# Performance work log

Measured on AMD Instinct MI355X. Metric: run time of the kernel, lower is better.

Reference implementation:

```python
import jax, jax.numpy as jnp
import numpy as np

N_NODES = 200000
N_EDGES = 6400000
N_LAYERS = 3
Z_DIM = 4  # 2*4 + 1 + 3 == 12 == Linear in_features


def setup_inputs() -> dict:
    key = jax.random.key(0)
    ks = jax.random.split(key, 7)
    z = jax.random.normal(ks[0], (N_NODES, Z_DIM), dtype=jnp.float32)
    r = jax.random.uniform(ks[1], (N_EDGES, 1), dtype=jnp.float32)
    r_hat = jax.random.normal(ks[2], (N_EDGES, 3), dtype=jnp.float32)
    # Per-layer Linear(12, 1) weights and biases, stacked over layers.
    W = jax.random.normal(ks[3], (N_LAYERS, 1, 12), dtype=jnp.float32) * (1.0 / np.sqrt(12.0))
    b = jnp.zeros((N_LAYERS, 1), dtype=jnp.float32)
    src = jax.random.randint(ks[4], (N_EDGES,), 0, N_NODES, dtype=jnp.int32)
    dst = jax.random.randint(ks[5], (N_EDGES,), 0, N_NODES, dtype=jnp.int32)
    return {"z": z, "r": r, "r_hat": r_hat, "W": W, "b": b, "src": src, "dst": dst}


def reference(z, r, r_hat, W, b, src, dst):
    # batch['x'] = batch['z'].copy()
    x = z
    n_nodes = z.shape[0]
    for i in range(W.shape[0]):
        # Per-edge gather + concat -> [E, 12]
        inpt = jnp.concatenate([z[src], z[dst], r, r_hat], axis=-1)
        # Tiny Linear(12, 1) -> per-edge scalar message [E, 1]
        msg = inpt @ W[i].T + b[i]
        # Scatter-sum messages onto destination nodes, residual update.
        agg = jax.ops.segment_sum(msg, dst, num_segments=n_nodes)  # [N, 1]
        z = z + agg  # broadcast over the 4 node features
    return z, x
```

## Files before the change

### kernel.cpp

```cpp
#include <hip/hip_runtime.h>

#define N_NODES 200000
#define N_EDGES 6400000
#define K_BUCKETS 256
#define BUCKET 784
#define NSB 1600
#define CHUNK 4000

__device__ __forceinline__ unsigned short f2bf(float x) {
    unsigned u = __float_as_uint(x);
    u += 0x7fffu + ((u >> 16) & 1u);
    return (unsigned short)(u >> 16);
}
__device__ __forceinline__ float bf2f(unsigned short h) {
    return __uint_as_float((unsigned)h << 16);
}


__global__ __launch_bounds__(256) void copy_x_prep(const float4* __restrict__ z,
                                                   float4* __restrict__ x_out,
                                                   float* __restrict__ Scum)
{
    int n = blockIdx.x * 256 + threadIdx.x;
    if (n < N_NODES) { x_out[n] = z[n]; Scum[n] = 0.0f; }
}

__global__ __launch_bounds__(256) void hist_kernel(const int* __restrict__ dst,
                                                   int* __restrict__ counts_T)
{
    __shared__ int cnt[K_BUCKETS];
    int tid = threadIdx.x, sb = blockIdx.x;
    cnt[tid] = 0;
    __syncthreads();
    int e0 = sb * CHUNK;
    for (int i = tid; i < CHUNK; i += 256)
        atomicAdd(&cnt[dst[e0 + i] / BUCKET], 1);
    __syncthreads();
    counts_T[(size_t)tid * NSB + sb] = cnt[tid];
}

__global__ __launch_bounds__(256) void scan_cols(const int* __restrict__ counts_T,
                                                 int* __restrict__ baseRel_T,
                                                 int* __restrict__ tot)
{
    __shared__ int buf[256];
    __shared__ int carry_s;
    int k = blockIdx.x, tid = threadIdx.x;
    if (tid == 0) carry_s = 0;
    __syncthreads();
    const int* col = counts_T + (size_t)k * NSB;
    int* outc = baseRel_T + (size_t)k * NSB;
    for (int base = 0; base < NSB; base += 256) {
        int idx = base + tid;
        int v = (idx < NSB) ? col[idx] : 0;
        buf[tid] = v;
        __syncthreads();
        for (int off = 1; off < 256; off <<= 1) {
            int t = (tid >= off) ? buf[tid - off] : 0;
            __syncthreads();
            buf[tid] += t;
            __syncthreads();
        }
        int incl = buf[tid];
        if (idx < NSB) outc[idx] = carry_s + incl - v;
        __syncthreads();
        if (tid == 255) carry_s += incl;
        __syncthreads();
    }
    if (tid == 255) tot[k] = carry_s;
}

__global__ __launch_bounds__(256) void scan_tot(const int* __restrict__ tot,
                                                int* __restrict__ bstart)
{
    __shared__ int buf[256];
    int tid = threadIdx.x;
    int v = tot[tid];
    buf[tid] = v;
    __syncthreads();
    for (int off = 1; off < 256; off <<= 1) {
        int t = (tid >= off) ? buf[tid - off] : 0;
        __syncthreads();
        buf[tid] += t;
        __syncthreads();
    }
    bstart[tid] = buf[tid] - v;
    if (tid == 255) bstart[256] = buf[255];
}

__global__ __launch_bounds__(256) void scatter_kernel(
    const int* __restrict__ src, const int* __restrict__ dst,
    const float* __restrict__ r, const float* __restrict__ r_hat,
    const float* __restrict__ W, const float* __restrict__ b,
    const int* __restrict__ baseRel_T, const int* __restrict__ bstart,
    int* __restrict__ packedA,
    unsigned short* __restrict__ c0a, unsigned short* __restrict__ c1a,
    unsigned short* __restrict__ c2a)
{
    __shared__ int cnt[K_BUCKETS];
    __shared__ int cur[K_BUCKETS];
    __shared__ int delta[K_BUCKETS];
    __shared__ int scanbuf[256];
    __shared__ int            lpack[CHUNK];
    __shared__ unsigned short lc0[CHUNK];
    __shared__ unsigned short lc1[CHUNK];
    __shared__ unsigned short lc2[CHUNK];
    __shared__ unsigned char  skb[CHUNK];

    int tid = threadIdx.x, sb = blockIdx.x;
    cnt[tid] = 0;
    __syncthreads();
    int e0 = sb * CHUNK;

    for (int i = tid; i < CHUNK; i += 256)
        atomicAdd(&cnt[dst[e0 + i] / BUCKET], 1);
    __syncthreads();

    int v = cnt[tid];
    scanbuf[tid] = v;
    __syncthreads();
    for (int off = 1; off < 256; off <<= 1) {
        int t = (tid >= off) ? scanbuf[tid - off] : 0;
        __syncthreads();
        scanbuf[tid] += t;
        __syncthreads();
    }
    int localBase = scanbuf[tid] - v;
    int gBase = bstart[tid] + baseRel_T[(size_t)tid * NSB + sb];
    delta[tid] = gBase - localBase;
    cur[tid] = localBase;
    __syncthreads();

    float w8_0 = W[8],  w9_0 = W[9],  w10_0 = W[10], w11_0 = W[11], b0 = b[0];
    float w8_1 = W[20], w9_1 = W[21], w10_1 = W[22], w11_1 = W[23], b1 = b[1];
    float w8_2 = W[32], w9_2 = W[33], w10_2 = W[34], w11_2 = W[35], b2 = b[2];

    for (int i = tid; i < CHUNK; i += 256) {
        int e = e0 + i;
        int d = dst[e];
        int k = d / BUCKET;
        int dl = d - k * BUCKET;
        int slot = atomicAdd(&cur[k], 1);
        int sn = src[e];
        float rv = r[e];
        size_t he = 3 * (size_t)e;
        float h0 = r_hat[he], h1 = r_hat[he + 1], h2 = r_hat[he + 2];
        lpack[slot] = (sn << 10) | dl;
        lc0[slot] = f2bf(w8_0 * rv + w9_0 * h0 + w10_0 * h1 + w11_0 * h2 + b0);
        lc1[slot] = f2bf(w8_1 * rv + w9_1 * h0 + w10_1 * h1 + w11_1 * h2 + b1);
        lc2[slot] = f2bf(w8_2 * rv + w9_2 * h0 + w10_2 * h1 + w11_2 * h2 + b2);
        skb[slot] = (unsigned char)k;
    }
    __syncthreads();

    for (int s = tid; s < CHUNK; s += 256) {
        int k = skb[s];
        int gpos = delta[k] + s;
        packedA[gpos] = lpack[s];
        c0a[gpos] = lc0[s];
        c1a[gpos] = lc1[s];
        c2a[gpos] = lc2[s];
    }
}

__global__ __launch_bounds__(256) void uv_kernel(
    const float4* __restrict__ z0, const float* __restrict__ Scum,
    const float* __restrict__ Wl,
    float* __restrict__ u, float* __restrict__ v)
{
    int n = blockIdx.x * 256 + threadIdx.x;
    if (n >= N_NODES) return;
    float a0 = Wl[0], a1 = Wl[1], a2 = Wl[2], a3 = Wl[3];
    float q0 = Wl[4], q1 = Wl[5], q2 = Wl[6], q3 = Wl[7];
    float A = a0 + a1 + a2 + a3, B = q0 + q1 + q2 + q3;
    float4 zv = z0[n];
    float S = Scum[n];
    u[n] = a0 * zv.x + a1 * zv.y + a2 * zv.z + a3 * zv.w + A * S;
    v[n] = q0 * zv.x + q1 * zv.y + q2 * zv.z + q3 * zv.w + B * S;
}

__global__ __launch_bounds__(1024) void layer_kernel(
    const int* __restrict__ packedA, const unsigned short* __restrict__ cpl,
    const int* __restrict__ bstart,
    const float* __restrict__ u, const float* __restrict__ v,
    float* __restrict__ Scum, int final_layer,
    const float4* __restrict__ z0, float4* __restrict__ z_out)
{
    __shared__ float vsl[BUCKET];
    __shared__ float aggsl[BUCKET];
    int tid = threadIdx.x, k = blockIdx.x;
    int nbase = k * BUCKET;
    int nn = min(BUCKET, N_NODES - nbase);

    for (int i = tid; i < nn; i += 1024) { vsl[i] = v[nbase + i]; aggsl[i] = 0.0f; }
    __syncthreads();

    int estart = bstart[k], eend = bstart[k + 1];
    for (int j = estart + tid; j < eend; j += 1024) {
        int pack = packedA[j];
        int s = pack >> 10;
        int dl = pack & 1023;
        float t = u[s] + vsl[dl] + bf2f(cpl[j]);
        atomicAdd(&aggsl[dl], t);
    }
    __syncthreads();

    for (int i = tid; i < nn; i += 1024) {
        float S = Scum[nbase + i] + aggsl[i];
        Scum[nbase + i] = S;
        if (final_layer) {
            float4 zv = z0[nbase + i];
            zv.x += S; zv.y += S; zv.z += S; zv.w += S;
            z_out[nbase + i] = zv;
        }
    }
}


__global__ __launch_bounds__(256) void init_kernel(
    const float4* __restrict__ z_in, float4* __restrict__ z_cur,
    float4* __restrict__ x_out, float* __restrict__ agg)
{
    int n = blockIdx.x * blockDim.x + threadIdx.x;
    if (n < N_NODES) {
        float4 vv = z_in[n];
        z_cur[n] = vv; x_out[n] = vv; agg[n] = 0.0f;
    }
}

__global__ __launch_bounds__(256) void edge_kernel(
    const float* __restrict__ z, const float* __restrict__ r,
    const float* __restrict__ r_hat, const int* __restrict__ src,
    const int* __restrict__ dst, const float* __restrict__ Wl,
    const float* __restrict__ bl, float* __restrict__ agg)
{
    int e = blockIdx.x * blockDim.x + threadIdx.x;
    if (e >= N_EDGES) return;
    float w0 = Wl[0], w1 = Wl[1], w2 = Wl[2], w3 = Wl[3];
    float w4 = Wl[4], w5 = Wl[5], w6 = Wl[6], w7 = Wl[7];
    float w8 = Wl[8], w9 = Wl[9], w10 = Wl[10], w11 = Wl[11];
    float bias = bl[0];
    int s = src[e], d = dst[e];
    float4 zs = ((const float4*)z)[s];
    float4 zd = ((const float4*)z)[d];
    float rv = r[e];
    const float* rh = r_hat + 3 * (size_t)e;
    float msg = w0*zs.x + w1*zs.y + w2*zs.z + w3*zs.w
              + w4*zd.x + w5*zd.y + w6*zd.z + w7*zd.w
              + w8*rv + w9*rh[0] + w10*rh[1] + w11*rh[2] + bias;
    unsafeAtomicAdd(&agg[d], msg);
}

__global__ __launch_bounds__(256) void node_update(float4* __restrict__ z_cur,
                                                   float* __restrict__ agg)
{
    int n = blockIdx.x * blockDim.x + threadIdx.x;
    if (n < N_NODES) {
        float a = agg[n]; float4 vv = z_cur[n];
        vv.x += a; vv.y += a; vv.z += a; vv.w += a;
        z_cur[n] = vv; agg[n] = 0.0f;
    }
}

__global__ __launch_bounds__(256) void final_update(const float4* __restrict__ z_cur,
                                                    const float* __restrict__ agg,
                                                    float4* __restrict__ z_out)
{
    int n = blockIdx.x * blockDim.x + threadIdx.x;
    if (n < N_NODES) {
        float a = agg[n]; float4 vv = z_cur[n];
        vv.x += a; vv.y += a; vv.z += a; vv.w += a;
        z_out[n] = vv;
    }
}


extern "C" void kernel_launch(void* const* d_in, const int* in_sizes, int n_in,
                              void* d_out, int out_size, void* d_ws, size_t ws_size,
                              hipStream_t stream)
{
    const float* z     = (const float*)d_in[0];
    const float* r     = (const float*)d_in[1];
    const float* r_hat = (const float*)d_in[2];
    const float* W     = (const float*)d_in[3];
    const float* b     = (const float*)d_in[4];
    const int*   src   = (const int*)d_in[5];
    const int*   dst   = (const int*)d_in[6];
    float* out = (float*)d_out;

    char* ws = (char*)d_ws;
    size_t off = 0;
    auto alloc = [&](size_t bytes) {
        void* p = ws + off;
        off += (bytes + 15) & ~(size_t)15;
        return p;
    };
    int*            packedA   = (int*)alloc((size_t)N_EDGES * 4);
    unsigned short* c0a       = (unsigned short*)alloc((size_t)N_EDGES * 2);
    unsigned short* c1a       = (unsigned short*)alloc((size_t)N_EDGES * 2);
    unsigned short* c2a       = (unsigned short*)alloc((size_t)N_EDGES * 2);
    int*            counts_T  = (int*)alloc((size_t)K_BUCKETS * NSB * 4);
    int*            baseRel_T = (int*)alloc((size_t)K_BUCKETS * NSB * 4);
    int*            tot       = (int*)alloc((size_t)K_BUCKETS * 4);
    int*            bstart    = (int*)alloc((size_t)(K_BUCKETS + 1) * 4);
    float*          Scum      = (float*)alloc((size_t)N_NODES * 4);
    float*          ubuf      = (float*)alloc((size_t)N_NODES * 4);
    float*          vbuf      = (float*)alloc((size_t)N_NODES * 4);
    size_t required = off;

    dim3 nblk((N_NODES + 255) / 256);

    if (ws_size >= required) {
        copy_x_prep<<<nblk, 256, 0, stream>>>(
            (const float4*)z, (float4*)(out + 4 * (size_t)N_NODES), Scum);
        hist_kernel<<<NSB, 256, 0, stream>>>(dst, counts_T);
        scan_cols<<<K_BUCKETS, 256, 0, stream>>>(counts_T, baseRel_T, tot);
        scan_tot<<<1, 256, 0, stream>>>(tot, bstart);
        scatter_kernel<<<NSB, 256, 0, stream>>>(src, dst, r, r_hat, W, b,
                                                baseRel_T, bstart,
                                                packedA, c0a, c1a, c2a);
        const unsigned short* cpl[3] = { c0a, c1a, c2a };
        for (int i = 0; i < 3; ++i) {
            uv_kernel<<<nblk, 256, 0, stream>>>(
                (const float4*)z, Scum, W + 12 * i, ubuf, vbuf);
            layer_kernel<<<K_BUCKETS, 1024, 0, stream>>>(
                packedA, cpl[i], bstart, ubuf, vbuf, Scum,
                (i == 2) ? 1 : 0, (const float4*)z, (float4*)out);
        }
    } else {
        float* agg   = (float*)d_ws;
        float* z_cur = agg + N_NODES;
        dim3 eblk((N_EDGES + 255) / 256);
        init_kernel<<<nblk, 256, 0, stream>>>(
            (const float4*)z, (float4*)z_cur,
            (float4*)(out + 4 * (size_t)N_NODES), agg);
        for (int i = 0; i < 3; ++i) {
            edge_kernel<<<eblk, 256, 0, stream>>>(
                z_cur, r, r_hat, src, dst, W + 12 * i, b + i, agg);
            if (i < 2)
                node_update<<<nblk, 256, 0, stream>>>((float4*)z_cur, agg);
            else
                final_update<<<nblk, 256, 0, stream>>>(
                    (const float4*)z_cur, agg, (float4*)out);
        }
    }
}
```

Measured before the change: 407.5 us.

## Split per-bucket aggregation across blocks with partial sums and fused node finalize

Each destination bucket's edge range is now processed by eight 256-thread blocks writing partial sums, replacing one 1024-thread block per bucket. A new finalize kernel reduces the partials and computes the next layer's u/v, which removes the separate uv kernel. The scatter kernel reuses the histogram counts instead of recounting, and the count/offset arrays switch to row-major. The first two layer coefficients are packed into one 32-bit word. Together these aim to raise occupancy in the aggregation phase and cut launches and redundant passes, at the cost of extra partial-buffer traffic and a change of CHUNK and NSB.

```diff
diff --git a/kernel.cpp b/kernel.cpp
--- a/kernel.cpp
+++ b/kernel.cpp
@@ -4,8 +4,9 @@
 #define N_EDGES 6400000
 #define K_BUCKETS 256
 #define BUCKET 784
-#define NSB 1600
-#define CHUNK 4000
+#define NSB 3200
+#define CHUNK 2000
+#define P_SPLIT 8
 
 __device__ __forceinline__ unsigned short f2bf(float x) {
     unsigned u = __float_as_uint(x);
@@ -17,16 +18,23 @@
 }
 
 
-__global__ __launch_bounds__(256) void copy_x_prep(const float4* __restrict__ z,
-                                                   float4* __restrict__ x_out,
-                                                   float* __restrict__ Scum)
+__global__ __launch_bounds__(256) void prep_kernel(
+    const float4* __restrict__ z, float4* __restrict__ x_out,
+    const float* __restrict__ W,
+    float* __restrict__ u, float* __restrict__ v)
 {
     int n = blockIdx.x * 256 + threadIdx.x;
-    if (n < N_NODES) { x_out[n] = z[n]; Scum[n] = 0.0f; }
+    if (n >= N_NODES) return;
+    float4 zv = z[n];
+    x_out[n] = zv;
+    float a0 = W[0], a1 = W[1], a2 = W[2], a3 = W[3];
+    float q0 = W[4], q1 = W[5], q2 = W[6], q3 = W[7];
+    u[n] = a0 * zv.x + a1 * zv.y + a2 * zv.z + a3 * zv.w;
+    v[n] = q0 * zv.x + q1 * zv.y + q2 * zv.z + q3 * zv.w;
 }
 
 __global__ __launch_bounds__(256) void hist_kernel(const int* __restrict__ dst,
-                                                   int* __restrict__ counts_T)
+                                                   int* __restrict__ counts)
 {
     __shared__ int cnt[K_BUCKETS];
     int tid = threadIdx.x, sb = blockIdx.x;
@@ -36,11 +44,11 @@
     for (int i = tid; i < CHUNK; i += 256)
         atomicAdd(&cnt[dst[e0 + i] / BUCKET], 1);
     __syncthreads();
-    counts_T[(size_t)tid * NSB + sb] = cnt[tid];
-}
-
-__global__ __launch_bounds__(256) void scan_cols(const int* __restrict__ counts_T,
-                                                 int* __restrict__ baseRel_T,
+    counts[sb * K_BUCKETS + tid] = cnt[tid];
+}
+
+__global__ __launch_bounds__(256) void scan_cols(const int* __restrict__ counts,
+                                                 int* __restrict__ baseRel,
                                                  int* __restrict__ tot)
 {
     __shared__ int buf[256];
@@ -48,11 +56,9 @@
     int k = blockIdx.x, tid = threadIdx.x;
     if (tid == 0) carry_s = 0;
     __syncthreads();
-    const int* col = counts_T + (size_t)k * NSB;
-    int* outc = baseRel_T + (size_t)k * NSB;
     for (int base = 0; base < NSB; base += 256) {
         int idx = base + tid;
-        int v = (idx < NSB) ? col[idx] : 0;
+        int v = (idx < NSB) ? counts[idx * K_BUCKETS + k] : 0;
         buf[tid] = v;
         __syncthreads();
         for (int off = 1; off < 256; off <<= 1) {
@@ -62,7 +68,7 @@
             __syncthreads();
         }
         int incl = buf[tid];
-        if (idx < NSB) outc[idx] = carry_s + incl - v;
+        if (idx < NSB) baseRel[idx * K_BUCKETS + k] = carry_s + incl - v;
         __syncthreads();
         if (tid == 255) carry_s += incl;
         __syncthreads();
@@ -92,31 +98,22 @@
     const int* __restrict__ src, const int* __restrict__ dst,
     const float* __restrict__ r, const float* __restrict__ r_hat,
     const float* __restrict__ W, const float* __restrict__ b,
-    const int* __restrict__ baseRel_T, const int* __restrict__ bstart,
-    int* __restrict__ packedA,
-    unsigned short* __restrict__ c0a, unsigned short* __restrict__ c1a,
+    const int* __restrict__ counts, const int* __restrict__ baseRel,
+    const int* __restrict__ bstart,
+    int* __restrict__ packedA, unsigned* __restrict__ c01a,
     unsigned short* __restrict__ c2a)
 {
-    __shared__ int cnt[K_BUCKETS];
     __shared__ int cur[K_BUCKETS];
     __shared__ int delta[K_BUCKETS];
     __shared__ int scanbuf[256];
     __shared__ int            lpack[CHUNK];
-    __shared__ unsigned short lc0[CHUNK];
-    __shared__ unsigned short lc1[CHUNK];
+    __shared__ unsigned       lc01[CHUNK];
     __shared__ unsigned short lc2[CHUNK];
     __shared__ unsigned char  skb[CHUNK];
 
     int tid = threadIdx.x, sb = blockIdx.x;
-    cnt[tid] = 0;
-    __syncthreads();
-    int e0 = sb * CHUNK;
-
-    for (int i = tid; i < CHUNK; i += 256)
-        atomicAdd(&cnt[dst[e0 + i] / BUCKET], 1);
-    __syncthreads();
-
-    int v = cnt[tid];
+
+    int v = counts[sb * K_BUCKETS + tid];
     scanbuf[tid] = v;
     __syncthreads();
     for (int off = 1; off < 256; off <<= 1) {
@@ -126,7 +123,7 @@
         __syncthreads();
     }
     int localBase = scanbuf[tid] - v;
-    int gBase = bstart[tid] + baseRel_T[(size_t)tid * NSB + sb];
+    int gBase = bstart[tid] + baseRel[sb * K_BUCKETS + tid];
     delta[tid] = gBase - localBase;
     cur[tid] = localBase;
     __syncthreads();
@@ -135,6 +132,7 @@
     float w8_1 = W[20], w9_1 = W[21], w10_1 = W[22], w11_1 = W[23], b1 = b[1];
     float w8_2 = W[32], w9_2 = W[33], w10_2 = W[34], w11_2 = W[35], b2 = b[2];
 
+    int e0 = sb * CHUNK;
     for (int i = tid; i < CHUNK; i += 256) {
         int e = e0 + i;
         int d = dst[e];
@@ -146,10 +144,11 @@
         size_t he = 3 * (size_t)e;
         float h0 = r_hat[he], h1 = r_hat[he + 1], h2 = r_hat[he + 2];
         lpack[slot] = (sn << 10) | dl;
-        lc0[slot] = f2bf(w8_0 * rv + w9_0 * h0 + w10_0 * h1 + w11_0 * h2 + b0);
-        lc1[slot] = f2bf(w8_1 * rv + w9_1 * h0 + w10_1 * h1 + w11_1 * h2 + b1);
-        lc2[slot] = f2bf(w8_2 * rv + w9_2 * h0 + w10_2 * h1 + w11_2 * h2 + b2);
-        skb[slot] = (unsigned char)k;
+        unsigned cc0 = f2bf(w8_0 * rv + w9_0 * h0 + w10_0 * h1 + w11_0 * h2 + b0);
+        unsigned cc1 = f2bf(w8_1 * rv + w9_1 * h0 + w10_1 * h1 + w11_1 * h2 + b1);
+        lc01[slot] = cc0 | (cc1 << 16);
+        lc2[slot]  = f2bf(w8_2 * rv + w9_2 * h0 + w10_2 * h1 + w11_2 * h2 + b2);
+        skb[slot]  = (unsigned char)k;
     }
     __syncthreads();
 
@@ -157,62 +156,79 @@
         int k = skb[s];
         int gpos = delta[k] + s;
         packedA[gpos] = lpack[s];
-        c0a[gpos] = lc0[s];
-        c1a[gpos] = lc1[s];
-        c2a[gpos] = lc2[s];
-    }
-}
-
-__global__ __launch_bounds__(256) void uv_kernel(
-    const float4* __restrict__ z0, const float* __restrict__ Scum,
-    const float* __restrict__ Wl,
-    float* __restrict__ u, float* __restrict__ v)
-{
-    int n = blockIdx.x * 256 + threadIdx.x;
-    if (n >= N_NODES) return;
-    float a0 = Wl[0], a1 = Wl[1], a2 = Wl[2], a3 = Wl[3];
-    float q0 = Wl[4], q1 = Wl[5], q2 = Wl[6], q3 = Wl[7];
-    float A = a0 + a1 + a2 + a3, B = q0 + q1 + q2 + q3;
-    float4 zv = z0[n];
-    float S = Scum[n];
-    u[n] = a0 * zv.x + a1 * zv.y + a2 * zv.z + a3 * zv.w + A * S;
-    v[n] = q0 * zv.x + q1 * zv.y + q2 * zv.z + q3 * zv.w + B * S;
-}
-
-__global__ __launch_bounds__(1024) void layer_kernel(
-    const int* __restrict__ packedA, const unsigned short* __restrict__ cpl,
-    const int* __restrict__ bstart,
+        c01a[gpos] = lc01[s];
+        c2a[gpos]  = lc2[s];
+    }
+}
+
+__global__ __launch_bounds__(256) void pagg_kernel(
+    const int* __restrict__ packedA, const unsigned* __restrict__ c01a,
+    const unsigned short* __restrict__ c2a, const int* __restrict__ bstart,
     const float* __restrict__ u, const float* __restrict__ v,
-    float* __restrict__ Scum, int final_layer,
-    const float4* __restrict__ z0, float4* __restrict__ z_out)
+    int layer, float* __restrict__ partial)
 {
     __shared__ float vsl[BUCKET];
     __shared__ float aggsl[BUCKET];
-    int tid = threadIdx.x, k = blockIdx.x;
+    int tid = threadIdx.x, blk = blockIdx.x;
+    int k = blk / P_SPLIT;
+    int p = blk - k * P_SPLIT;
     int nbase = k * BUCKET;
     int nn = min(BUCKET, N_NODES - nbase);
 
-    for (int i = tid; i < nn; i += 1024) { vsl[i] = v[nbase + i]; aggsl[i] = 0.0f; }
+    for (int i = tid; i < BUCKET; i += 256) {
+        aggsl[i] = 0.0f;
+        vsl[i] = (i < nn) ? v[nbase + i] : 0.0f;
+    }
     __syncthreads();
 
     int estart = bstart[k], eend = bstart[k + 1];
-    for (int j = estart + tid; j < eend; j += 1024) {
+    int len = eend - estart;
+    int per = (len + P_SPLIT - 1) / P_SPLIT;
+    int lo = estart + p * per;
+    int hi = min(lo + per, eend);
+
+    for (int j = lo + tid; j < hi; j += 256) {
         int pack = packedA[j];
         int s = pack >> 10;
         int dl = pack & 1023;
-        float t = u[s] + vsl[dl] + bf2f(cpl[j]);
-        atomicAdd(&aggsl[dl], t);
-    }
-    __syncthreads();
-
-    for (int i = tid; i < nn; i += 1024) {
-        float S = Scum[nbase + i] + aggsl[i];
-        Scum[nbase + i] = S;
-        if (final_layer) {
-            float4 zv = z0[nbase + i];
-            zv.x += S; zv.y += S; zv.z += S; zv.w += S;
-            z_out[nbase + i] = zv;
-        }
+        float c = (layer == 2) ? bf2f(c2a[j])
+                               : bf2f((unsigned short)(c01a[j] >> (16 * layer)));
+        atomicAdd(&aggsl[dl], u[s] + vsl[dl] + c);
+    }
+    __syncthreads();
+
+    float* pout = partial + (size_t)blk * BUCKET;
+    for (int i = tid; i < BUCKET; i += 256) pout[i] = aggsl[i];
+}
+
+__global__ __launch_bounds__(256) void fin_kernel(
+    const float4* __restrict__ z0, const float* __restrict__ partial,
+    const float* __restrict__ Sin, float* __restrict__ Sout,
+    const float* __restrict__ W, int layer,
+    float* __restrict__ u, float* __restrict__ v, float4* __restrict__ z_out)
+{
+    int n = blockIdx.x * 256 + threadIdx.x;
+    if (n >= N_NODES) return;
+    int k = n / BUCKET;
+    int i = n - k * BUCKET;
+    float agg = 0.0f;
+    const float* pk = partial + (size_t)k * P_SPLIT * BUCKET + i;
+#pragma unroll
+    for (int p = 0; p < P_SPLIT; ++p) agg += pk[(size_t)p * BUCKET];
+    float S = ((layer == 0) ? 0.0f : Sin[n]) + agg;
+    if (layer < 2) {
+        const float* Wn = W + 12 * (layer + 1);
+        float a0 = Wn[0], a1 = Wn[1], a2 = Wn[2], a3 = Wn[3];
+        float q0 = Wn[4], q1 = Wn[5], q2 = Wn[6], q3 = Wn[7];
+        float A = a0 + a1 + a2 + a3, B = q0 + q1 + q2 + q3;
+        float4 zv = z0[n];
+        Sout[n] = S;
+        u[n] = a0 * zv.x + a1 * zv.y + a2 * zv.z + a3 * zv.w + A * S;
+        v[n] = q0 * zv.x + q1 * zv.y + q2 * zv.z + q3 * zv.w + B * S;
+    } else {
+        float4 zv = z0[n];
+        zv.x += S; zv.y += S; zv.z += S; zv.w += S;
+        z_out[n] = zv;
     }
 }
 
@@ -295,38 +311,43 @@
         off += (bytes + 15) & ~(size_t)15;
         return p;
     };
-    int*            packedA   = (int*)alloc((size_t)N_EDGES * 4);
-    unsigned short* c0a       = (unsigned short*)alloc((size_t)N_EDGES * 2);
-    unsigned short* c1a       = (unsigned short*)alloc((size_t)N_EDGES * 2);
-    unsigned short* c2a       = (unsigned short*)alloc((size_t)N_EDGES * 2);
-    int*            counts_T  = (int*)alloc((size_t)K_BUCKETS * NSB * 4);
-    int*            baseRel_T = (int*)alloc((size_t)K_BUCKETS * NSB * 4);
-    int*            tot       = (int*)alloc((size_t)K_BUCKETS * 4);
-    int*            bstart    = (int*)alloc((size_t)(K_BUCKETS + 1) * 4);
-    float*          Scum      = (float*)alloc((size_t)N_NODES * 4);
-    float*          ubuf      = (float*)alloc((size_t)N_NODES * 4);
-    float*          vbuf      = (float*)alloc((size_t)N_NODES * 4);
+    int*            packedA = (int*)alloc((size_t)N_EDGES * 4);
+    unsigned*       c01a    = (unsigned*)alloc((size_t)N_EDGES * 4);
+    unsigned short* c2a     = (unsigned short*)alloc((size_t)N_EDGES * 2);
+    int*            counts  = (int*)alloc((size_t)NSB * K_BUCKETS * 4);
+    int*            baseRel = (int*)alloc((size_t)NSB * K_BUCKETS * 4);
+    int*            tot     = (int*)alloc((size_t)K_BUCKETS * 4);
+    int*            bstart  = (int*)alloc((size_t)(K_BUCKETS + 1) * 4);
+    float*          Sa      = (float*)alloc((size_t)N_NODES * 4);
+    float*          Sb      = (float*)alloc((size_t)N_NODES * 4);
+    float*          ubuf    = (float*)alloc((size_t)N_NODES * 4);
+    float*          vbuf    = (float*)alloc((size_t)N_NODES * 4);
+    float*          partial = (float*)alloc((size_t)K_BUCKETS * P_SPLIT * BUCKET * 4);
     size_t required = off;
 
     dim3 nblk((N_NODES + 255) / 256);
 
     if (ws_size >= required) {
-        copy_x_prep<<<nblk, 256, 0, stream>>>(
-            (const float4*)z, (float4*)(out + 4 * (size_t)N_NODES), Scum);
-        hist_kernel<<<NSB, 256, 0, stream>>>(dst, counts_T);
-        scan_cols<<<K_BUCKETS, 256, 0, stream>>>(counts_T, baseRel_T, tot);
+        prep_kernel<<<nblk, 256, 0, stream>>>(
+            (const float4*)z, (float4*)(out + 4 * (size_t)N_NODES), W, ubuf, vbuf);
+        hist_kernel<<<NSB, 256, 0, stream>>>(dst, counts);
+        scan_cols<<<K_BUCKETS, 256, 0, stream>>>(counts, baseRel, tot);
         scan_tot<<<1, 256, 0, stream>>>(tot, bstart);
         scatter_kernel<<<NSB, 256, 0, stream>>>(src, dst, r, r_hat, W, b,
-                                                baseRel_T, bstart,
-                                                packedA, c0a, c1a, c2a);
-        const unsigned short* cpl[3] = { c0a, c1a, c2a };
-        for (int i = 0; i < 3; ++i) {
-            uv_kernel<<<nblk, 256, 0, stream>>>(
-                (const float4*)z, Scum, W + 12 * i, ubuf, vbuf);
-            layer_kernel<<<K_BUCKETS, 1024, 0, stream>>>(
-                packedA, cpl[i], bstart, ubuf, vbuf, Scum,
-                (i == 2) ? 1 : 0, (const float4*)z, (float4*)out);
-        }
+                                                counts, baseRel, bstart,
+                                                packedA, c01a, c2a);
+        pagg_kernel<<<K_BUCKETS * P_SPLIT, 256, 0, stream>>>(
+            packedA, c01a, c2a, bstart, ubuf, vbuf, 0, partial);
+        fin_kernel<<<nblk, 256, 0, stream>>>(
+            (const float4*)z, partial, Sa, Sa, W, 0, ubuf, vbuf, (float4*)out);
+        pagg_kernel<<<K_BUCKETS * P_SPLIT, 256, 0, stream>>>(
+            packedA, c01a, c2a, bstart, ubuf, vbuf, 1, partial);
+        fin_kernel<<<nblk, 256, 0, stream>>>(
+            (const float4*)z, partial, Sa, Sb, W, 1, ubuf, vbuf, (float4*)out);
+        pagg_kernel<<<K_BUCKETS * P_SPLIT, 256, 0, stream>>>(
+            packedA, c01a, c2a, bstart, ubuf, vbuf, 2, partial);
+        fin_kernel<<<nblk, 256, 0, stream>>>(
+            (const float4*)z, partial, Sb, Sb, W, 2, ubuf, vbuf, (float4*)out);
     } else {
         float* agg   = (float*)d_ws;
         float* z_cur = agg + N_NODES;
```

Result: no change. 403.5 us (-1.0%).
